# Kernel tuning notes

Hardware: AMD Instinct MI355X
Metric: run time of the kernel (lower is better)

The kernel has to match this reference:

```python
import jax, jax.numpy as jnp
import numpy as np

B, S, D, H = 8, 1024, 512, 8
HD = D // H
NEG = -1000000000.0
LN_EPS = 1e-5


def setup_inputs() -> dict:
    key = jax.random.key(0)
    ks = jax.random.split(key, 16)
    sc = 0.02
    inp = {
        "query": jax.random.normal(ks[0], (B, S, D), jnp.float32),
        "inputs": jax.random.normal(ks[1], (B, S, D), jnp.float32),
        "ren_mat": jax.random.uniform(ks[2], (B, S, S), jnp.float32) * 5.0,
        "timestamp": jax.random.normal(ks[3], (B, S, S), jnp.float32),
        # causal mask: True where attention is disallowed (strictly upper triangular)
        "mask": jnp.triu(jnp.ones((1, S, S), jnp.bool_), k=1),
        "Wq": jax.random.normal(ks[4], (D, D), jnp.float32) * sc,
        "bq": jnp.zeros((D,), jnp.float32),
        "Wk": jax.random.normal(ks[5], (D, D), jnp.float32) * sc,
        "bk": jnp.zeros((D,), jnp.float32),
        "Wv": jax.random.normal(ks[6], (D, D), jnp.float32) * sc,
        "bv": jnp.zeros((D,), jnp.float32),
        "Wo": jax.random.normal(ks[7], (D, D), jnp.float32) * sc,
        "bo": jnp.zeros((D,), jnp.float32),
        "W1": jax.random.normal(ks[8], (D, D), jnp.float32) * sc,
        "b1": jnp.zeros((D,), jnp.float32),
        "ln_g": jnp.ones((D,), jnp.float32),
        "ln_b": jnp.zeros((D,), jnp.float32),
        "l1": jax.random.uniform(ks[9], (1,), jnp.float32),
    }
    return inp


def reference(query, inputs, ren_mat, timestamp, mask,
              Wq, bq, Wk, bk, Wv, bv, Wo, bo, W1, b1, ln_g, ln_b, l1):
    # QKV projections (qk_same=False path; q,k,v all computed from `inputs`)
    def proj(x, W, b):
        return (x @ W.T + b).reshape(B, S, H, HD).transpose(0, 2, 1, 3)  # (B,H,S,HD)

    q = proj(inputs, Wq, bq)
    k = proj(inputs, Wk, bk)
    v = proj(inputs, Wv, bv)

    m = mask[:, None]  # (1,1,S,S), broadcasts over batch & heads

    scores = jnp.einsum("bhqd,bhkd->bhqk", q, k) / jnp.sqrt(jnp.float32(HD))
    scores = jnp.where(m, NEG, scores)
    prob_attn = jax.nn.softmax(scores, axis=-1)

    # memory blend: log10(ren+1) and exp(-|t|), each masked, summed, softmaxed
    ren_feat = jnp.where(m, NEG, jnp.log10(ren_mat + 1.0)[:, None])      # (B,H,S,S)
    time_stamp = jnp.where(m, NEG, jnp.exp(-jnp.abs(timestamp))[:, None])
    mem_attn = jax.nn.softmax(ren_feat + time_stamp, axis=-1)

    l = l1  # (1,) learned blend coefficient
    prob_attn = (1.0 - l) * prob_attn + l * mem_attn

    out = jnp.einsum("bhqk,bhkd->bhqd", prob_attn, v)
    out = out.transpose(0, 2, 1, 3).reshape(B, S, D)
    out = out @ Wo.T + bo

    # residual FFN + layernorm (dropout disabled / eval mode)
    out = out + (out @ W1.T + b1)
    mu = jnp.mean(out, axis=-1, keepdims=True)
    var = jnp.var(out, axis=-1, keepdims=True)
    out = (out - mu) / jnp.sqrt(var + LN_EPS) * ln_g + ln_b
    return out
```

## Files before the change

### kernel.cpp

```cpp
#include <hip/hip_runtime.h>
#include <math.h>

constexpr int kB = 8, kS = 1024, kD = 512, kH = 8, kHD = 64;
constexpr int kM = kB * kS;

typedef __attribute__((ext_vector_type(8))) short s8v;
typedef __attribute__((ext_vector_type(4))) float f4v;
typedef __attribute__((ext_vector_type(4))) unsigned short u4v;

__device__ __forceinline__ unsigned short f2bf(float f) {
    union { float f; unsigned int u; } c; c.f = f;
    unsigned int u = c.u + 0x7FFFu + ((c.u >> 16) & 1u);
    return (unsigned short)(u >> 16);
}

__device__ __forceinline__ void gl2lds(const unsigned short* g, unsigned short* l) {
    __builtin_amdgcn_global_load_lds(
        (const __attribute__((address_space(1))) unsigned int*)g,
        (__attribute__((address_space(3))) unsigned int*)l, 16, 0, 0);
}

__global__ __launch_bounds__(256) void cvt_kernel(
    const float* __restrict__ X, const float* __restrict__ Wq,
    const float* __restrict__ Wk, const float* __restrict__ Wv,
    const float* __restrict__ Wo, const float* __restrict__ W1,
    unsigned short* __restrict__ Xbf, unsigned short* __restrict__ Wqkv,
    unsigned short* __restrict__ Wobf, unsigned short* __restrict__ W1bf)
{
    const int idx = blockIdx.x * 256 + threadIdx.x;
    const float* src; unsigned short* dst; int off;
    if (idx < 1048576)      { src = X;  dst = Xbf;           off = idx; }
    else if (idx < 1114112) { src = Wq; dst = Wqkv;          off = idx - 1048576; }
    else if (idx < 1179648) { src = Wk; dst = Wqkv + 262144; off = idx - 1114112; }
    else if (idx < 1245184) { src = Wv; dst = Wqkv + 524288; off = idx - 1179648; }
    else if (idx < 1310720) { src = Wo; dst = Wobf;          off = idx - 1245184; }
    else                    { src = W1; dst = W1bf;          off = idx - 1310720; }
    const float4 v = ((const float4*)src)[off];
    u4v p;
    p[0] = f2bf(v.x); p[1] = f2bf(v.y); p[2] = f2bf(v.z); p[3] = f2bf(v.w);
    ((u4v*)dst)[off] = p;
}

__device__ __forceinline__ void mfma_core(
    const unsigned short* __restrict__ A, const unsigned short* __restrict__ B,
    unsigned short* As, unsigned short* Bs, f4v acc[4][4])
{
    const int M0 = blockIdx.x * 128, N0 = blockIdx.y * 128;
    const int t = threadIdx.x, w = t >> 6, lane = t & 63;
    const int l16 = lane & 15, quad = lane >> 4;
    const int wm = (w & 1) * 64, wn = (w >> 1) * 64;

    const unsigned short* gA[2]; const unsigned short* gB[2];
    unsigned short* lA[2]; unsigned short* lB[2];
#pragma unroll
    for (int i = 0; i < 2; ++i) {
        const int r0 = w * 32 + i * 16;
        const int r = r0 + (lane >> 2);
        const int c = (lane & 3) ^ ((r >> 1) & 3);
        gA[i] = A + (size_t)(M0 + r) * 512 + c * 8;
        gB[i] = B + (size_t)(N0 + r) * 512 + c * 8;
        lA[i] = As + r0 * 32;
        lB[i] = Bs + r0 * 32;
    }

    const f4v zero = {0.0f, 0.0f, 0.0f, 0.0f};
#pragma unroll
    for (int mt = 0; mt < 4; ++mt)
#pragma unroll
        for (int nt = 0; nt < 4; ++nt) acc[mt][nt] = zero;

#pragma unroll 1
    for (int k0 = 0; k0 < 512; k0 += 32) {
        gl2lds(gA[0] + k0, lA[0]);
        gl2lds(gA[1] + k0, lA[1]);
        gl2lds(gB[0] + k0, lB[0]);
        gl2lds(gB[1] + k0, lB[1]);
        __syncthreads();
        s8v af[4], bf_[4];
#pragma unroll
        for (int mt = 0; mt < 4; ++mt) {
            const int r = wm + mt * 16 + l16;
            const int p = r * 4 + (quad ^ ((r >> 1) & 3));
            af[mt] = *(const s8v*)&As[p * 8];
        }
#pragma unroll
        for (int nt = 0; nt < 4; ++nt) {
            const int r = wn + nt * 16 + l16;
            const int p = r * 4 + (quad ^ ((r >> 1) & 3));
            bf_[nt] = *(const s8v*)&Bs[p * 8];
        }
#pragma unroll
        for (int mt = 0; mt < 4; ++mt)
#pragma unroll
            for (int nt = 0; nt < 4; ++nt)
                acc[mt][nt] = __builtin_amdgcn_mfma_f32_16x16x32_bf16(
                    af[mt], bf_[nt], acc[mt][nt], 0, 0, 0);
        __syncthreads();
    }
}

__global__ __launch_bounds__(256) void qkv_mfma_kernel(
    const unsigned short* __restrict__ Xbf, const unsigned short* __restrict__ Wqkv,
    const float* __restrict__ bq, const float* __restrict__ bk, const float* __restrict__ bv,
    unsigned short* __restrict__ qbf, unsigned short* __restrict__ kbf,
    unsigned short* __restrict__ vTbf)
{
    __shared__ __align__(16) unsigned short As[128 * 32];
    __shared__ __align__(16) unsigned short Bs[128 * 32];
    f4v acc[4][4];
    mfma_core(Xbf, Wqkv, As, Bs, acc);

    const int M0 = blockIdx.x * 128, N0 = blockIdx.y * 128;
    const int t = threadIdx.x, w = t >> 6, lane = t & 63;
    const int l16 = lane & 15, quad = lane >> 4;
    const int wm = (w & 1) * 64, wn = (w >> 1) * 64;
    const int z = N0 >> 9;
    const float* bias = (z == 0) ? bq : (z == 1) ? bk : bv;

    if (z <= 1) {
        unsigned short* out = (z == 0) ? qbf : kbf;
#pragma unroll
        for (int nt = 0; nt < 4; ++nt) {
            const int n512 = (N0 + wn + nt * 16 + l16) & 511;
            const int h = n512 >> 6, hd = n512 & 63;
            const float bv_ = bias[n512];
#pragma unroll
            for (int mt = 0; mt < 4; ++mt) {
#pragma unroll
                for (int rr = 0; rr < 4; ++rr) {
                    const int m = M0 + wm + mt * 16 + quad * 4 + rr;
                    const int b = m >> 10, s = m & (kS - 1);
                    out[(((size_t)b * kH + h) * kS + s) * kHD + hd] =
                        f2bf(acc[mt][nt][rr] + bv_);
                }
            }
        }
    } else {
#pragma unroll
        for (int nt = 0; nt < 4; ++nt) {
            const int n512 = (N0 + wn + nt * 16 + l16) & 511;
            const int h = n512 >> 6, hd = n512 & 63;
            const float bv_ = bias[n512];
#pragma unroll
            for (int mt = 0; mt < 4; ++mt) {
                const int m0_ = M0 + wm + mt * 16 + quad * 4;
                const int b = m0_ >> 10, s = m0_ & (kS - 1);
                u4v pk;
#pragma unroll
                for (int rr = 0; rr < 4; ++rr) pk[rr] = f2bf(acc[mt][nt][rr] + bv_);
                *(u4v*)(vTbf + (((size_t)b * kH + h) * kHD + hd) * kS + s) = pk;
            }
        }
    }
}

__global__ __launch_bounds__(256) void gemm_wo_kernel(
    const unsigned short* __restrict__ Abf, const unsigned short* __restrict__ Wobf,
    const float* __restrict__ bo, float* __restrict__ out1f,
    unsigned short* __restrict__ out1bf)
{
    __shared__ __align__(16) unsigned short As[128 * 32];
    __shared__ __align__(16) unsigned short Bs[128 * 32];
    f4v acc[4][4];
    mfma_core(Abf, Wobf, As, Bs, acc);

    const int M0 = blockIdx.x * 128, N0 = blockIdx.y * 128;
    const int t = threadIdx.x, w = t >> 6, lane = t & 63;
    const int l16 = lane & 15, quad = lane >> 4;
    const int wm = (w & 1) * 64, wn = (w >> 1) * 64;
#pragma unroll
    for (int nt = 0; nt < 4; ++nt) {
        const int n = N0 + wn + nt * 16 + l16;
        const float bv_ = bo[n];
#pragma unroll
        for (int mt = 0; mt < 4; ++mt) {
#pragma unroll
            for (int rr = 0; rr < 4; ++rr) {
                const int m = M0 + wm + mt * 16 + quad * 4 + rr;
                const float val = acc[mt][nt][rr] + bv_;
                out1f[(size_t)m * kD + n] = val;
                out1bf[(size_t)m * kD + n] = f2bf(val);
            }
        }
    }
}

__global__ __launch_bounds__(256) void gemm_w1_kernel(
    const unsigned short* __restrict__ Abf, const unsigned short* __restrict__ W1bf,
    const float* __restrict__ b1, const float* __restrict__ resid,
    float* __restrict__ out)
{
    __shared__ __align__(16) unsigned short As[128 * 32];
    __shared__ __align__(16) unsigned short Bs[128 * 32];
    f4v acc[4][4];
    mfma_core(Abf, W1bf, As, Bs, acc);

    const int M0 = blockIdx.x * 128, N0 = blockIdx.y * 128;
    const int t = threadIdx.x, w = t >> 6, lane = t & 63;
    const int l16 = lane & 15, quad = lane >> 4;
    const int wm = (w & 1) * 64, wn = (w >> 1) * 64;
#pragma unroll
    for (int nt = 0; nt < 4; ++nt) {
        const int n = N0 + wn + nt * 16 + l16;
        const float bv_ = b1[n];
#pragma unroll
        for (int mt = 0; mt < 4; ++mt) {
#pragma unroll
            for (int rr = 0; rr < 4; ++rr) {
                const int m = M0 + wm + mt * 16 + quad * 4 + rr;
                out[(size_t)m * kD + n] = acc[mt][nt][rr] + bv_ + resid[(size_t)m * kD + n];
            }
        }
    }
}

__global__ __launch_bounds__(256) void mem_softmax_kernel(
    const float* __restrict__ ren, const float* __restrict__ ts,
    unsigned short* __restrict__ mem)
{
    const int bi = blockIdx.x;
    const int i = bi & (kS - 1);
    const float* renr = ren + (size_t)bi * kS;
    const float* tsr  = ts  + (size_t)bi * kS;
    unsigned short* memr = mem + (size_t)bi * kS;
    const int t = threadIdx.x;
    const int j0 = t * 4;
    __shared__ float red[4];

    const float4 r4 = *(const float4*)(renr + j0);
    const float4 t4 = *(const float4*)(tsr + j0);
    float rv[4] = {r4.x, r4.y, r4.z, r4.w};
    float tv[4] = {t4.x, t4.y, t4.z, t4.w};
    float p4[4];
    float lsum = 0.0f;
#pragma unroll
    for (int e = 0; e < 4; ++e) {
        const int j = j0 + e;
        float p = 0.0f;
        if (j <= i) {
            const float val = 0.30102999566f * __log2f(rv[e] + 1.0f) + __expf(-fabsf(tv[e]));
            p = __expf(val);
        }
        p4[e] = p;
        lsum += p;
    }
#pragma unroll
    for (int d = 1; d < 64; d <<= 1) lsum += __shfl_xor(lsum, d);
    if ((t & 63) == 0) red[t >> 6] = lsum;
    __syncthreads();
    const float Z = red[0] + red[1] + red[2] + red[3];
    const float inv = 1.0f / Z;
    u4v pk;
#pragma unroll
    for (int e = 0; e < 4; ++e) pk[e] = f2bf(p4[e] * inv);
    *(u4v*)(memr + j0) = pk;
}

#define LDSFRAG(tile, r, c) (*(const s8v*)&(tile)[(size_t)(r) * 64 + ((((c) ^ ((r) & 7))) << 3)])

__global__ __launch_bounds__(256) void flash_attn_kernel(
    const unsigned short* __restrict__ q, const unsigned short* __restrict__ k,
    const unsigned short* __restrict__ vT, const unsigned short* __restrict__ mem,
    const float* __restrict__ l1, unsigned short* __restrict__ aout)
{
    const int qt = 15 - blockIdx.x;
    const int h = blockIdx.y, b = blockIdx.z;
    const int bh = b * kH + h;
    const int t = threadIdx.x;
    const int w = t >> 6, lane = t & 63;
    const int quad = lane >> 4, l16 = lane & 15;
    const int r0 = qt * 64 + w * 16;
    const float lam = l1[0];

    __shared__ __align__(16) unsigned short KV[2][2][64 * 64];
    __shared__ __align__(16) unsigned short P_lds[4][16][72];

    const unsigned short* qrow = q + ((size_t)bh * kS + r0 + l16) * kHD;
    const s8v qa0 = *(const s8v*)(qrow + quad * 8);
    const s8v qa1 = *(const s8v*)(qrow + 32 + quad * 8);

    const unsigned short* kb = k + (size_t)bh * kS * kHD;
    const unsigned short* vb = vT + (size_t)bh * kHD * kS;
    const unsigned short* mb = mem + ((size_t)b * kS + r0 + l16) * kS;

    const unsigned short* gsrc[4];
    int gstep[4];
    unsigned short* ldst[4];
#pragma unroll
    for (int u = 0; u < 4; ++u) {
        const int s = w * 4 + u;
        const int rloc = (s & 7) * 8 + (lane >> 3);
        const int chunk = (lane & 7) ^ ((lane >> 3) & 7);
        if (s < 8) {
            gsrc[u] = kb + (size_t)rloc * kHD + chunk * 8;
            gstep[u] = kHD;
            ldst[u] = &KV[0][0][(size_t)s * 512];
        } else {
            gsrc[u] = vb + (size_t)rloc * kS + chunk * 8;
            gstep[u] = 1;
            ldst[u] = &KV[0][1][(size_t)(s - 8) * 512];
        }
    }

#pragma unroll
    for (int u = 0; u < 4; ++u) gl2lds(gsrc[u], ldst[u]);
    s8v ma0_c = *(const s8v*)(mb + quad * 8);
    s8v ma1_c = *(const s8v*)(mb + 32 + quad * 8);

    const f4v zero = {0.0f, 0.0f, 0.0f, 0.0f};
    float l_run[4] = {0.0f, 0.0f, 0.0f, 0.0f};
    f4v Oa[4], Om[4];
#pragma unroll
    for (int nt = 0; nt < 4; ++nt) { Oa[nt] = zero; Om[nt] = zero; }

    for (int kt = 0; kt <= qt; ++kt) {
        __syncthreads();
        const int cur = kt & 1;
        s8v ma0_n, ma1_n;
        if (kt < qt) {
            const int jn = (kt + 1) * 64;
            const int boff = ((kt + 1) & 1) * 8192;
#pragma unroll
            for (int u = 0; u < 4; ++u)
                gl2lds(gsrc[u] + (size_t)jn * gstep[u], ldst[u] + boff);
            ma0_n = *(const s8v*)(mb + jn + quad * 8);
            ma1_n = *(const s8v*)(mb + jn + 32 + quad * 8);
        }
        const unsigned short* Kc = &KV[cur][0][0];
        const unsigned short* Vc = &KV[cur][1][0];
        const int j0 = kt * 64;

#pragma unroll
        for (int ct = 0; ct < 4; ++ct) {
            const int r = ct * 16 + l16;
            const s8v kb0 = LDSFRAG(Kc, r, quad);
            const s8v kb1 = LDSFRAG(Kc, r, 4 + quad);
            f4v acc = zero;
            acc = __builtin_amdgcn_mfma_f32_16x16x32_bf16(qa0, kb0, acc, 0, 0, 0);
            acc = __builtin_amdgcn_mfma_f32_16x16x32_bf16(qa1, kb1, acc, 0, 0, 0);
            const int j = j0 + r;
#pragma unroll
            for (int rr = 0; rr < 4; ++rr) {
                float p = __expf(acc[rr] * 0.125f);
                if (kt == qt && j > r0 + quad * 4 + rr) p = 0.0f;
                l_run[rr] += p;
                P_lds[w][quad * 4 + rr][ct * 16 + l16] = f2bf(p);
            }
        }
        const s8v pa0 = *(const s8v*)&P_lds[w][l16][quad * 8];
        const s8v pa1 = *(const s8v*)&P_lds[w][l16][32 + quad * 8];
#pragma unroll
        for (int nt = 0; nt < 4; ++nt) {
            const int r = nt * 16 + l16;
            const s8v vb0 = LDSFRAG(Vc, r, quad);
            const s8v vb1 = LDSFRAG(Vc, r, 4 + quad);
            Oa[nt] = __builtin_amdgcn_mfma_f32_16x16x32_bf16(pa0, vb0, Oa[nt], 0, 0, 0);
            Oa[nt] = __builtin_amdgcn_mfma_f32_16x16x32_bf16(pa1, vb1, Oa[nt], 0, 0, 0);
            Om[nt] = __builtin_amdgcn_mfma_f32_16x16x32_bf16(ma0_c, vb0, Om[nt], 0, 0, 0);
            Om[nt] = __builtin_amdgcn_mfma_f32_16x16x32_bf16(ma1_c, vb1, Om[nt], 0, 0, 0);
        }
        if (kt < qt) { ma0_c = ma0_n; ma1_c = ma1_n; }
    }
    float inv[4];
#pragma unroll
    for (int rr = 0; rr < 4; ++rr) {
        float Z = l_run[rr];
        Z += __shfl_xor(Z, 1);
        Z += __shfl_xor(Z, 2);
        Z += __shfl_xor(Z, 4);
        Z += __shfl_xor(Z, 8);
        inv[rr] = (1.0f - lam) / Z;
    }
#pragma unroll
    for (int nt = 0; nt < 4; ++nt)
#pragma unroll
        for (int rr = 0; rr < 4; ++rr) {
            const int i = r0 + quad * 4 + rr;
            const int d = h * kHD + nt * 16 + l16;
            aout[((size_t)b * kS + i) * kD + d] =
                f2bf(Oa[nt][rr] * inv[rr] + lam * Om[nt][rr]);
        }
}

__global__ __launch_bounds__(256) void ln_kernel(
    const float* __restrict__ x, const float* __restrict__ g,
    const float* __restrict__ bb, float* __restrict__ out)
{
    const int row = blockIdx.x;
    const int t = threadIdx.x;
    const float* xr = x + (size_t)row * kD;
    float a = xr[t], c = xr[t + 256];
    __shared__ float red[256];
    float s1 = a + c, s2 = a * a + c * c;
    red[t] = s1;
    __syncthreads();
    for (int s = 128; s > 0; s >>= 1) {
        if (t < s) red[t] += red[t + s];
        __syncthreads();
    }
    const float sum = red[0];
    __syncthreads();
    red[t] = s2;
    __syncthreads();
    for (int s = 128; s > 0; s >>= 1) {
        if (t < s) red[t] += red[t + s];
        __syncthreads();
    }
    const float sq = red[0];
    float mu = sum * (1.0f / kD);
    float var = sq * (1.0f / kD) - mu * mu;
    float inv = rsqrtf(var + 1e-5f);
    out[(size_t)row * kD + t]       = (a - mu) * inv * g[t] + bb[t];
    out[(size_t)row * kD + t + 256] = (c - mu) * inv * g[t + 256] + bb[t + 256];
}

extern "C" void kernel_launch(void* const* d_in, const int* in_sizes, int n_in,
                              void* d_out, int out_size, void* d_ws, size_t ws_size,
                              hipStream_t stream) {
    const float* X   = (const float*)d_in[1];
    const float* ren = (const float*)d_in[2];
    const float* ts  = (const float*)d_in[3];
    const float* Wq = (const float*)d_in[5];  const float* bq = (const float*)d_in[6];
    const float* Wk = (const float*)d_in[7];  const float* bk = (const float*)d_in[8];
    const float* Wv = (const float*)d_in[9];  const float* bv = (const float*)d_in[10];
    const float* Wo = (const float*)d_in[11]; const float* bo = (const float*)d_in[12];
    const float* W1 = (const float*)d_in[13]; const float* b1 = (const float*)d_in[14];
    const float* lng = (const float*)d_in[15]; const float* lnb = (const float*)d_in[16];
    const float* l1 = (const float*)d_in[17];
    float* out = (float*)d_out;

    char* wsb = (char*)d_ws;
    unsigned short* Xbf    = (unsigned short*)(wsb);
    unsigned short* Wqkvbf = (unsigned short*)(wsb + (8u  << 20));
    unsigned short* Wobf   = (unsigned short*)(wsb + (10u << 20));
    unsigned short* W1bf   = (unsigned short*)(wsb + (11u << 20));
    unsigned short* qbf    = (unsigned short*)(wsb + (12u << 20));
    unsigned short* kbf    = (unsigned short*)(wsb + (20u << 20));
    unsigned short* vTbf   = (unsigned short*)(wsb + (28u << 20));
    unsigned short* membf  = (unsigned short*)(wsb + (36u << 20));
    unsigned short* aoutbf = (unsigned short*)(wsb + (52u << 20));
    float*          out1f  = (float*)(wsb + (60u << 20));
    unsigned short* out1bf = (unsigned short*)(wsb + (76u << 20));

    cvt_kernel<<<dim3(5376), 256, 0, stream>>>(
        X, Wq, Wk, Wv, Wo, W1, Xbf, Wqkvbf, Wobf, W1bf);
    qkv_mfma_kernel<<<dim3(kM / 128, 1536 / 128), 256, 0, stream>>>(
        Xbf, Wqkvbf, bq, bk, bv, qbf, kbf, vTbf);
    mem_softmax_kernel<<<dim3(kB * kS), 256, 0, stream>>>(ren, ts, membf);
    flash_attn_kernel<<<dim3(kS / 64, kH, kB), 256, 0, stream>>>(
        qbf, kbf, vTbf, membf, l1, aoutbf);
    gemm_wo_kernel<<<dim3(kM / 128, kD / 128), 256, 0, stream>>>(
        aoutbf, Wobf, bo, out1f, out1bf);
    gemm_w1_kernel<<<dim3(kM / 128, kD / 128), 256, 0, stream>>>(
        out1bf, W1bf, b1, out1f, out);
    ln_kernel<<<dim3(kM), 256, 0, stream>>>(out, lng, lnb, out);
}
```

Baseline: 283.2 us.

## Fuse prep kernels, fold residual into W1, pair causal tiles in attention

Merges the weight/input conversion and the memory-softmax into one launch. Adds the identity to W1 so the residual is computed inside the GEMM, which removes the fp32 out1 buffer and its reads. The V projection is computed transposed so each store goes directly into the vT layout. Flash attention now gives each block one high and one low query tile to balance causal work, sharing K/V loads and halving the grid. The Wo and W1 GEMMs switch to 128x64 tiles to launch more blocks. Folding the residual into bf16 W1 rounds the identity term to bf16, which adds precision risk.

```diff
diff --git a/kernel.cpp b/kernel.cpp
--- a/kernel.cpp
+++ b/kernel.cpp
@@ -20,46 +20,98 @@
         (__attribute__((address_space(3))) unsigned int*)l, 16, 0, 0);
 }
 
-__global__ __launch_bounds__(256) void cvt_kernel(
+__global__ __launch_bounds__(256) void prep_kernel(
     const float* __restrict__ X, const float* __restrict__ Wq,
     const float* __restrict__ Wk, const float* __restrict__ Wv,
     const float* __restrict__ Wo, const float* __restrict__ W1,
+    const float* __restrict__ ren, const float* __restrict__ ts,
     unsigned short* __restrict__ Xbf, unsigned short* __restrict__ Wqkv,
-    unsigned short* __restrict__ Wobf, unsigned short* __restrict__ W1bf)
-{
-    const int idx = blockIdx.x * 256 + threadIdx.x;
-    const float* src; unsigned short* dst; int off;
-    if (idx < 1048576)      { src = X;  dst = Xbf;           off = idx; }
-    else if (idx < 1114112) { src = Wq; dst = Wqkv;          off = idx - 1048576; }
-    else if (idx < 1179648) { src = Wk; dst = Wqkv + 262144; off = idx - 1114112; }
-    else if (idx < 1245184) { src = Wv; dst = Wqkv + 524288; off = idx - 1179648; }
-    else if (idx < 1310720) { src = Wo; dst = Wobf;          off = idx - 1245184; }
-    else                    { src = W1; dst = W1bf;          off = idx - 1310720; }
-    const float4 v = ((const float4*)src)[off];
-    u4v p;
-    p[0] = f2bf(v.x); p[1] = f2bf(v.y); p[2] = f2bf(v.z); p[3] = f2bf(v.w);
-    ((u4v*)dst)[off] = p;
-}
-
-__device__ __forceinline__ void mfma_core(
+    unsigned short* __restrict__ Wobf, unsigned short* __restrict__ W1bf,
+    unsigned short* __restrict__ mem)
+{
+    __shared__ float red[4];
+    const int t = threadIdx.x;
+    if (blockIdx.x < 5376) {
+        const int idx = blockIdx.x * 256 + t;
+        const float* src; unsigned short* dst; int off; bool isw1 = false;
+        if (idx < 1048576)      { src = X;  dst = Xbf;           off = idx; }
+        else if (idx < 1114112) { src = Wq; dst = Wqkv;          off = idx - 1048576; }
+        else if (idx < 1179648) { src = Wk; dst = Wqkv + 262144; off = idx - 1114112; }
+        else if (idx < 1245184) { src = Wv; dst = Wqkv + 524288; off = idx - 1179648; }
+        else if (idx < 1310720) { src = Wo; dst = Wobf;          off = idx - 1245184; }
+        else                    { src = W1; dst = W1bf;          off = idx - 1310720; isw1 = true; }
+        float4 v = ((const float4*)src)[off];
+        if (isw1) {
+            const int e0 = off * 4;
+            const int row = e0 >> 9, col0 = e0 & 511;
+            if (row >= col0 && row < col0 + 4) ((float*)&v)[row - col0] += 1.0f;
+        }
+        u4v p;
+        p[0] = f2bf(v.x); p[1] = f2bf(v.y); p[2] = f2bf(v.z); p[3] = f2bf(v.w);
+        ((u4v*)dst)[off] = p;
+        return;
+    }
+    const int bi = blockIdx.x - 5376;
+    const int i = bi & (kS - 1);
+    const float* renr = ren + (size_t)bi * kS;
+    const float* tsr  = ts  + (size_t)bi * kS;
+    unsigned short* memr = mem + (size_t)bi * kS;
+    const int j0 = t * 4;
+    const float4 r4 = *(const float4*)(renr + j0);
+    const float4 t4 = *(const float4*)(tsr + j0);
+    float rv[4] = {r4.x, r4.y, r4.z, r4.w};
+    float tv[4] = {t4.x, t4.y, t4.z, t4.w};
+    float p4[4];
+    float lsum = 0.0f;
+#pragma unroll
+    for (int e = 0; e < 4; ++e) {
+        const int j = j0 + e;
+        float p = 0.0f;
+        if (j <= i) {
+            const float val = 0.30102999566f * __log2f(rv[e] + 1.0f) + __expf(-fabsf(tv[e]));
+            p = __expf(val);
+        }
+        p4[e] = p;
+        lsum += p;
+    }
+#pragma unroll
+    for (int d = 1; d < 64; d <<= 1) lsum += __shfl_xor(lsum, d);
+    if ((t & 63) == 0) red[t >> 6] = lsum;
+    __syncthreads();
+    const float Z = red[0] + red[1] + red[2] + red[3];
+    const float inv = 1.0f / Z;
+    u4v pk;
+#pragma unroll
+    for (int e = 0; e < 4; ++e) pk[e] = f2bf(p4[e] * inv);
+    *(u4v*)(memr + j0) = pk;
+}
+
+template <int NT>
+__device__ __forceinline__ void mfma_core2(
     const unsigned short* __restrict__ A, const unsigned short* __restrict__ B,
-    unsigned short* As, unsigned short* Bs, f4v acc[4][4])
-{
-    const int M0 = blockIdx.x * 128, N0 = blockIdx.y * 128;
+    int M0, int N0, unsigned short* As, unsigned short* Bs, f4v (&acc)[4][NT])
+{
     const int t = threadIdx.x, w = t >> 6, lane = t & 63;
     const int l16 = lane & 15, quad = lane >> 4;
-    const int wm = (w & 1) * 64, wn = (w >> 1) * 64;
-
-    const unsigned short* gA[2]; const unsigned short* gB[2];
-    unsigned short* lA[2]; unsigned short* lB[2];
+    const int wm = (w & 1) * 64, wn = (w >> 1) * (NT * 16);
+    constexpr int NB = NT / 2;
+
+    const unsigned short* gA[2]; unsigned short* lA[2];
 #pragma unroll
     for (int i = 0; i < 2; ++i) {
         const int r0 = w * 32 + i * 16;
         const int r = r0 + (lane >> 2);
         const int c = (lane & 3) ^ ((r >> 1) & 3);
         gA[i] = A + (size_t)(M0 + r) * 512 + c * 8;
+        lA[i] = As + r0 * 32;
+    }
+    const unsigned short* gB[NB]; unsigned short* lB[NB];
+#pragma unroll
+    for (int i = 0; i < NB; ++i) {
+        const int r0 = w * (16 * NB) + i * 16;
+        const int r = r0 + (lane >> 2);
+        const int c = (lane & 3) ^ ((r >> 1) & 3);
         gB[i] = B + (size_t)(N0 + r) * 512 + c * 8;
-        lA[i] = As + r0 * 32;
         lB[i] = Bs + r0 * 32;
     }
 
@@ -67,16 +119,16 @@
 #pragma unroll
     for (int mt = 0; mt < 4; ++mt)
 #pragma unroll
-        for (int nt = 0; nt < 4; ++nt) acc[mt][nt] = zero;
+        for (int nt = 0; nt < NT; ++nt) acc[mt][nt] = zero;
 
 #pragma unroll 1
     for (int k0 = 0; k0 < 512; k0 += 32) {
         gl2lds(gA[0] + k0, lA[0]);
         gl2lds(gA[1] + k0, lA[1]);
-        gl2lds(gB[0] + k0, lB[0]);
-        gl2lds(gB[1] + k0, lB[1]);
+#pragma unroll
+        for (int i = 0; i < NB; ++i) gl2lds(gB[i] + k0, lB[i]);
         __syncthreads();
-        s8v af[4], bf_[4];
+        s8v af[4], bf_[NT];
 #pragma unroll
         for (int mt = 0; mt < 4; ++mt) {
             const int r = wm + mt * 16 + l16;
@@ -84,7 +136,7 @@
             af[mt] = *(const s8v*)&As[p * 8];
         }
 #pragma unroll
-        for (int nt = 0; nt < 4; ++nt) {
+        for (int nt = 0; nt < NT; ++nt) {
             const int r = wn + nt * 16 + l16;
             const int p = r * 4 + (quad ^ ((r >> 1) & 3));
             bf_[nt] = *(const s8v*)&Bs[p * 8];
@@ -92,7 +144,7 @@
 #pragma unroll
         for (int mt = 0; mt < 4; ++mt)
 #pragma unroll
-            for (int nt = 0; nt < 4; ++nt)
+            for (int nt = 0; nt < NT; ++nt)
                 acc[mt][nt] = __builtin_amdgcn_mfma_f32_16x16x32_bf16(
                     af[mt], bf_[nt], acc[mt][nt], 0, 0, 0);
         __syncthreads();
@@ -108,16 +160,16 @@
     __shared__ __align__(16) unsigned short As[128 * 32];
     __shared__ __align__(16) unsigned short Bs[128 * 32];
     f4v acc[4][4];
-    mfma_core(Xbf, Wqkv, As, Bs, acc);
-
-    const int M0 = blockIdx.x * 128, N0 = blockIdx.y * 128;
+    const int y = blockIdx.y;
     const int t = threadIdx.x, w = t >> 6, lane = t & 63;
     const int l16 = lane & 15, quad = lane >> 4;
     const int wm = (w & 1) * 64, wn = (w >> 1) * 64;
-    const int z = N0 >> 9;
-    const float* bias = (z == 0) ? bq : (z == 1) ? bk : bv;
-
-    if (z <= 1) {
+
+    if (y < 8) {
+        const int M0 = blockIdx.x * 128, N0 = y * 128;
+        mfma_core2<4>(Xbf, Wqkv, M0, N0, As, Bs, acc);
+        const int z = N0 >> 9;
+        const float* bias = (z == 0) ? bq : bk;
         unsigned short* out = (z == 0) ? qbf : kbf;
 #pragma unroll
         for (int nt = 0; nt < 4; ++nt) {
@@ -136,19 +188,22 @@
             }
         }
     } else {
-#pragma unroll
-        for (int nt = 0; nt < 4; ++nt) {
-            const int n512 = (N0 + wn + nt * 16 + l16) & 511;
-            const int h = n512 >> 6, hd = n512 & 63;
-            const float bv_ = bias[n512];
-#pragma unroll
-            for (int mt = 0; mt < 4; ++mt) {
-                const int m0_ = M0 + wm + mt * 16 + quad * 4;
-                const int b = m0_ >> 10, s = m0_ & (kS - 1);
-                u4v pk;
-#pragma unroll
-                for (int rr = 0; rr < 4; ++rr) pk[rr] = f2bf(acc[mt][nt][rr] + bv_);
-                *(u4v*)(vTbf + (((size_t)b * kH + h) * kHD + hd) * kS + s) = pk;
+        const int M0 = (y - 8) * 128, N0 = blockIdx.x * 128;
+        mfma_core2<4>(Wqkv + (size_t)1024 * 512, Xbf, M0, N0, As, Bs, acc);
+#pragma unroll
+        for (int mt = 0; mt < 4; ++mt) {
+#pragma unroll
+            for (int rr = 0; rr < 4; ++rr) {
+                const int vcol = M0 + wm + mt * 16 + quad * 4 + rr;
+                const int h = vcol >> 6, hd = vcol & 63;
+                const float bv_ = bv[vcol];
+#pragma unroll
+                for (int nt = 0; nt < 4; ++nt) {
+                    const int sg = N0 + wn + nt * 16 + l16;
+                    const int b = sg >> 10, s = sg & (kS - 1);
+                    vTbf[(((size_t)b * kH + h) * kHD + hd) * kS + s] =
+                        f2bf(acc[mt][nt][rr] + bv_);
+                }
             }
         }
     }
@@ -156,104 +211,54 @@
 
 __global__ __launch_bounds__(256) void gemm_wo_kernel(
     const unsigned short* __restrict__ Abf, const unsigned short* __restrict__ Wobf,
-    const float* __restrict__ bo, float* __restrict__ out1f,
-    unsigned short* __restrict__ out1bf)
+    const float* __restrict__ bo, unsigned short* __restrict__ out1bf)
 {
     __shared__ __align__(16) unsigned short As[128 * 32];
-    __shared__ __align__(16) unsigned short Bs[128 * 32];
-    f4v acc[4][4];
-    mfma_core(Abf, Wobf, As, Bs, acc);
-
-    const int M0 = blockIdx.x * 128, N0 = blockIdx.y * 128;
+    __shared__ __align__(16) unsigned short Bs[64 * 32];
+    f4v acc[4][2];
+    const int M0 = blockIdx.x * 128, N0 = blockIdx.y * 64;
+    mfma_core2<2>(Abf, Wobf, M0, N0, As, Bs, acc);
     const int t = threadIdx.x, w = t >> 6, lane = t & 63;
     const int l16 = lane & 15, quad = lane >> 4;
-    const int wm = (w & 1) * 64, wn = (w >> 1) * 64;
-#pragma unroll
-    for (int nt = 0; nt < 4; ++nt) {
+    const int wm = (w & 1) * 64, wn = (w >> 1) * 32;
+#pragma unroll
+    for (int nt = 0; nt < 2; ++nt) {
         const int n = N0 + wn + nt * 16 + l16;
         const float bv_ = bo[n];
 #pragma unroll
-        for (int mt = 0; mt < 4; ++mt) {
+        for (int mt = 0; mt < 4; ++mt)
 #pragma unroll
             for (int rr = 0; rr < 4; ++rr) {
                 const int m = M0 + wm + mt * 16 + quad * 4 + rr;
-                const float val = acc[mt][nt][rr] + bv_;
-                out1f[(size_t)m * kD + n] = val;
-                out1bf[(size_t)m * kD + n] = f2bf(val);
-            }
-        }
+                out1bf[(size_t)m * kD + n] = f2bf(acc[mt][nt][rr] + bv_);
+            }
     }
 }
 
 __global__ __launch_bounds__(256) void gemm_w1_kernel(
     const unsigned short* __restrict__ Abf, const unsigned short* __restrict__ W1bf,
-    const float* __restrict__ b1, const float* __restrict__ resid,
-    float* __restrict__ out)
+    const float* __restrict__ b1, float* __restrict__ out)
 {
     __shared__ __align__(16) unsigned short As[128 * 32];
-    __shared__ __align__(16) unsigned short Bs[128 * 32];
-    f4v acc[4][4];
-    mfma_core(Abf, W1bf, As, Bs, acc);
-
-    const int M0 = blockIdx.x * 128, N0 = blockIdx.y * 128;
+    __shared__ __align__(16) unsigned short Bs[64 * 32];
+    f4v acc[4][2];
+    const int M0 = blockIdx.x * 128, N0 = blockIdx.y * 64;
+    mfma_core2<2>(Abf, W1bf, M0, N0, As, Bs, acc);
     const int t = threadIdx.x, w = t >> 6, lane = t & 63;
     const int l16 = lane & 15, quad = lane >> 4;
-    const int wm = (w & 1) * 64, wn = (w >> 1) * 64;
-#pragma unroll
-    for (int nt = 0; nt < 4; ++nt) {
+    const int wm = (w & 1) * 64, wn = (w >> 1) * 32;
+#pragma unroll
+    for (int nt = 0; nt < 2; ++nt) {
         const int n = N0 + wn + nt * 16 + l16;
         const float bv_ = b1[n];
 #pragma unroll
-        for (int mt = 0; mt < 4; ++mt) {
+        for (int mt = 0; mt < 4; ++mt)
 #pragma unroll
             for (int rr = 0; rr < 4; ++rr) {
                 const int m = M0 + wm + mt * 16 + quad * 4 + rr;
-                out[(size_t)m * kD + n] = acc[mt][nt][rr] + bv_ + resid[(size_t)m * kD + n];
-            }
-        }
-    }
-}
-
-__global__ __launch_bounds__(256) void mem_softmax_kernel(
-    const float* __restrict__ ren, const float* __restrict__ ts,
-    unsigned short* __restrict__ mem)
-{
-    const int bi = blockIdx.x;
-    const int i = bi & (kS - 1);
-    const float* renr = ren + (size_t)bi * kS;
-    const float* tsr  = ts  + (size_t)bi * kS;
-    unsigned short* memr = mem + (size_t)bi * kS;
-    const int t = threadIdx.x;
-    const int j0 = t * 4;
-    __shared__ float red[4];
-
-    const float4 r4 = *(const float4*)(renr + j0);
-    const float4 t4 = *(const float4*)(tsr + j0);
-    float rv[4] = {r4.x, r4.y, r4.z, r4.w};
-    float tv[4] = {t4.x, t4.y, t4.z, t4.w};
-    float p4[4];
-    float lsum = 0.0f;
-#pragma unroll
-    for (int e = 0; e < 4; ++e) {
-        const int j = j0 + e;
-        float p = 0.0f;
-        if (j <= i) {
-            const float val = 0.30102999566f * __log2f(rv[e] + 1.0f) + __expf(-fabsf(tv[e]));
-            p = __expf(val);
-        }
-        p4[e] = p;
-        lsum += p;
-    }
-#pragma unroll
-    for (int d = 1; d < 64; d <<= 1) lsum += __shfl_xor(lsum, d);
-    if ((t & 63) == 0) red[t >> 6] = lsum;
-    __syncthreads();
-    const float Z = red[0] + red[1] + red[2] + red[3];
-    const float inv = 1.0f / Z;
-    u4v pk;
-#pragma unroll
-    for (int e = 0; e < 4; ++e) pk[e] = f2bf(p4[e] * inv);
-    *(u4v*)(memr + j0) = pk;
+                out[(size_t)m * kD + n] = acc[mt][nt][rr] + bv_;
+            }
+    }
 }
 
 #define LDSFRAG(tile, r, c) (*(const s8v*)&(tile)[(size_t)(r) * 64 + ((((c) ^ ((r) & 7))) << 3)])
@@ -263,25 +268,31 @@
     const unsigned short* __restrict__ vT, const unsigned short* __restrict__ mem,
     const float* __restrict__ l1, unsigned short* __restrict__ aout)
 {
-    const int qt = 15 - blockIdx.x;
+    const int qp = blockIdx.x;
+    const int hi = 15 - qp, lo = qp;
     const int h = blockIdx.y, b = blockIdx.z;
     const int bh = b * kH + h;
     const int t = threadIdx.x;
     const int w = t >> 6, lane = t & 63;
     const int quad = lane >> 4, l16 = lane & 15;
-    const int r0 = qt * 64 + w * 16;
     const float lam = l1[0];
 
     __shared__ __align__(16) unsigned short KV[2][2][64 * 64];
     __shared__ __align__(16) unsigned short P_lds[4][16][72];
 
-    const unsigned short* qrow = q + ((size_t)bh * kS + r0 + l16) * kHD;
-    const s8v qa0 = *(const s8v*)(qrow + quad * 8);
-    const s8v qa1 = *(const s8v*)(qrow + 32 + quad * 8);
+    const int tbase[2] = {hi * 64, lo * 64};
+    s8v qa[2][2];
+    const unsigned short* mbase[2];
+#pragma unroll
+    for (int ti = 0; ti < 2; ++ti) {
+        const unsigned short* qrow = q + ((size_t)bh * kS + tbase[ti] + w * 16 + l16) * kHD;
+        qa[ti][0] = *(const s8v*)(qrow + quad * 8);
+        qa[ti][1] = *(const s8v*)(qrow + 32 + quad * 8);
+        mbase[ti] = mem + ((size_t)b * kS + tbase[ti] + w * 16 + l16) * kS;
+    }
 
     const unsigned short* kb = k + (size_t)bh * kS * kHD;
     const unsigned short* vb = vT + (size_t)bh * kHD * kS;
-    const unsigned short* mb = mem + ((size_t)b * kS + r0 + l16) * kS;
 
     const unsigned short* gsrc[4];
     int gstep[4];
@@ -304,82 +315,111 @@
 
 #pragma unroll
     for (int u = 0; u < 4; ++u) gl2lds(gsrc[u], ldst[u]);
-    s8v ma0_c = *(const s8v*)(mb + quad * 8);
-    s8v ma1_c = *(const s8v*)(mb + 32 + quad * 8);
+    s8v maC[2][2];
+#pragma unroll
+    for (int ti = 0; ti < 2; ++ti) {
+        maC[ti][0] = *(const s8v*)(mbase[ti] + quad * 8);
+        maC[ti][1] = *(const s8v*)(mbase[ti] + 32 + quad * 8);
+    }
 
     const f4v zero = {0.0f, 0.0f, 0.0f, 0.0f};
-    float l_run[4] = {0.0f, 0.0f, 0.0f, 0.0f};
-    f4v Oa[4], Om[4];
-#pragma unroll
-    for (int nt = 0; nt < 4; ++nt) { Oa[nt] = zero; Om[nt] = zero; }
-
-    for (int kt = 0; kt <= qt; ++kt) {
+    f4v Oa[2][4], Om[2][4];
+    float lr[2][4];
+#pragma unroll
+    for (int ti = 0; ti < 2; ++ti)
+#pragma unroll
+        for (int nt = 0; nt < 4; ++nt) {
+            Oa[ti][nt] = zero; Om[ti][nt] = zero; lr[ti][nt] = 0.0f;
+        }
+
+    for (int kt = 0; kt <= hi; ++kt) {
         __syncthreads();
         const int cur = kt & 1;
-        s8v ma0_n, ma1_n;
-        if (kt < qt) {
+        s8v maN[2][2];
+        const bool stage_next = (kt < hi);
+        if (stage_next) {
             const int jn = (kt + 1) * 64;
             const int boff = ((kt + 1) & 1) * 8192;
 #pragma unroll
             for (int u = 0; u < 4; ++u)
                 gl2lds(gsrc[u] + (size_t)jn * gstep[u], ldst[u] + boff);
-            ma0_n = *(const s8v*)(mb + jn + quad * 8);
-            ma1_n = *(const s8v*)(mb + jn + 32 + quad * 8);
+            maN[0][0] = *(const s8v*)(mbase[0] + jn + quad * 8);
+            maN[0][1] = *(const s8v*)(mbase[0] + jn + 32 + quad * 8);
+            if (kt + 1 <= lo) {
+                maN[1][0] = *(const s8v*)(mbase[1] + jn + quad * 8);
+                maN[1][1] = *(const s8v*)(mbase[1] + jn + 32 + quad * 8);
+            }
         }
         const unsigned short* Kc = &KV[cur][0][0];
         const unsigned short* Vc = &KV[cur][1][0];
-        const int j0 = kt * 64;
-
-#pragma unroll
-        for (int ct = 0; ct < 4; ++ct) {
-            const int r = ct * 16 + l16;
-            const s8v kb0 = LDSFRAG(Kc, r, quad);
-            const s8v kb1 = LDSFRAG(Kc, r, 4 + quad);
-            f4v acc = zero;
-            acc = __builtin_amdgcn_mfma_f32_16x16x32_bf16(qa0, kb0, acc, 0, 0, 0);
-            acc = __builtin_amdgcn_mfma_f32_16x16x32_bf16(qa1, kb1, acc, 0, 0, 0);
-            const int j = j0 + r;
-#pragma unroll
-            for (int rr = 0; rr < 4; ++rr) {
-                float p = __expf(acc[rr] * 0.125f);
-                if (kt == qt && j > r0 + quad * 4 + rr) p = 0.0f;
-                l_run[rr] += p;
-                P_lds[w][quad * 4 + rr][ct * 16 + l16] = f2bf(p);
-            }
-        }
-        const s8v pa0 = *(const s8v*)&P_lds[w][l16][quad * 8];
-        const s8v pa1 = *(const s8v*)&P_lds[w][l16][32 + quad * 8];
+
+        s8v vf[4][2];
 #pragma unroll
         for (int nt = 0; nt < 4; ++nt) {
             const int r = nt * 16 + l16;
-            const s8v vb0 = LDSFRAG(Vc, r, quad);
-            const s8v vb1 = LDSFRAG(Vc, r, 4 + quad);
-            Oa[nt] = __builtin_amdgcn_mfma_f32_16x16x32_bf16(pa0, vb0, Oa[nt], 0, 0, 0);
-            Oa[nt] = __builtin_amdgcn_mfma_f32_16x16x32_bf16(pa1, vb1, Oa[nt], 0, 0, 0);
-            Om[nt] = __builtin_amdgcn_mfma_f32_16x16x32_bf16(ma0_c, vb0, Om[nt], 0, 0, 0);
-            Om[nt] = __builtin_amdgcn_mfma_f32_16x16x32_bf16(ma1_c, vb1, Om[nt], 0, 0, 0);
-        }
-        if (kt < qt) { ma0_c = ma0_n; ma1_c = ma1_n; }
-    }
-    float inv[4];
-#pragma unroll
-    for (int rr = 0; rr < 4; ++rr) {
-        float Z = l_run[rr];
-        Z += __shfl_xor(Z, 1);
-        Z += __shfl_xor(Z, 2);
-        Z += __shfl_xor(Z, 4);
-        Z += __shfl_xor(Z, 8);
-        inv[rr] = (1.0f - lam) / Z;
-    }
-#pragma unroll
-    for (int nt = 0; nt < 4; ++nt)
+            vf[nt][0] = LDSFRAG(Vc, r, quad);
+            vf[nt][1] = LDSFRAG(Vc, r, 4 + quad);
+        }
+
+#pragma unroll
+        for (int ti = 0; ti < 2; ++ti) {
+            if (ti == 1 && kt > lo) continue;
+            const bool diag = (kt == ((ti == 0) ? hi : lo));
+#pragma unroll
+            for (int ct = 0; ct < 4; ++ct) {
+                const int r = ct * 16 + l16;
+                const s8v kb0 = LDSFRAG(Kc, r, quad);
+                const s8v kb1 = LDSFRAG(Kc, r, 4 + quad);
+                f4v acc = zero;
+                acc = __builtin_amdgcn_mfma_f32_16x16x32_bf16(qa[ti][0], kb0, acc, 0, 0, 0);
+                acc = __builtin_amdgcn_mfma_f32_16x16x32_bf16(qa[ti][1], kb1, acc, 0, 0, 0);
+#pragma unroll
+                for (int rr = 0; rr < 4; ++rr) {
+                    float p = __expf(acc[rr] * 0.125f);
+                    if (diag && (ct * 16 + l16) > (w * 16 + quad * 4 + rr)) p = 0.0f;
+                    lr[ti][rr] += p;
+                    P_lds[w][quad * 4 + rr][ct * 16 + l16] = f2bf(p);
+                }
+            }
+            const s8v pa0 = *(const s8v*)&P_lds[w][l16][quad * 8];
+            const s8v pa1 = *(const s8v*)&P_lds[w][l16][32 + quad * 8];
+#pragma unroll
+            for (int nt = 0; nt < 4; ++nt) {
+                Oa[ti][nt] = __builtin_amdgcn_mfma_f32_16x16x32_bf16(pa0, vf[nt][0], Oa[ti][nt], 0, 0, 0);
+                Oa[ti][nt] = __builtin_amdgcn_mfma_f32_16x16x32_bf16(pa1, vf[nt][1], Oa[ti][nt], 0, 0, 0);
+                Om[ti][nt] = __builtin_amdgcn_mfma_f32_16x16x32_bf16(maC[ti][0], vf[nt][0], Om[ti][nt], 0, 0, 0);
+                Om[ti][nt] = __builtin_amdgcn_mfma_f32_16x16x32_bf16(maC[ti][1], vf[nt][1], Om[ti][nt], 0, 0, 0);
+            }
+        }
+        if (stage_next) {
+            maC[0][0] = maN[0][0]; maC[0][1] = maN[0][1];
+            if (kt + 1 <= lo) { maC[1][0] = maN[1][0]; maC[1][1] = maN[1][1]; }
+        }
+    }
+
+#pragma unroll
+    for (int ti = 0; ti < 2; ++ti) {
+        float inv[4];
 #pragma unroll
         for (int rr = 0; rr < 4; ++rr) {
-            const int i = r0 + quad * 4 + rr;
-            const int d = h * kHD + nt * 16 + l16;
-            aout[((size_t)b * kS + i) * kD + d] =
-                f2bf(Oa[nt][rr] * inv[rr] + lam * Om[nt][rr]);
-        }
+            float Z = lr[ti][rr];
+            Z += __shfl_xor(Z, 1);
+            Z += __shfl_xor(Z, 2);
+            Z += __shfl_xor(Z, 4);
+            Z += __shfl_xor(Z, 8);
+            inv[rr] = (1.0f - lam) / Z;
+        }
+        const int r0 = tbase[ti] + w * 16;
+#pragma unroll
+        for (int nt = 0; nt < 4; ++nt)
+#pragma unroll
+            for (int rr = 0; rr < 4; ++rr) {
+                const int i = r0 + quad * 4 + rr;
+                const int d = h * kHD + nt * 16 + l16;
+                aout[((size_t)b * kS + i) * kD + d] =
+                    f2bf(Oa[ti][nt][rr] * inv[rr] + lam * Om[ti][nt][rr]);
+            }
+    }
 }
 
 __global__ __launch_bounds__(256) void ln_kernel(
@@ -439,19 +479,17 @@
     unsigned short* vTbf   = (unsigned short*)(wsb + (28u << 20));
     unsigned short* membf  = (unsigned short*)(wsb + (36u << 20));
     unsigned short* aoutbf = (unsigned short*)(wsb + (52u << 20));
-    float*          out1f  = (float*)(wsb + (60u << 20));
-    unsigned short* out1bf = (unsigned short*)(wsb + (76u << 20));
-
-    cvt_kernel<<<dim3(5376), 256, 0, stream>>>(
-        X, Wq, Wk, Wv, Wo, W1, Xbf, Wqkvbf, Wobf, W1bf);
-    qkv_mfma_kernel<<<dim3(kM / 128, 1536 / 128), 256, 0, stream>>>(
+    unsigned short* out1bf = (unsigned short*)(wsb + (60u << 20));
+
+    prep_kernel<<<dim3(5376 + kB * kS), 256, 0, stream>>>(
+        X, Wq, Wk, Wv, Wo, W1, ren, ts, Xbf, Wqkvbf, Wobf, W1bf, membf);
+    qkv_mfma_kernel<<<dim3(kM / 128, 12), 256, 0, stream>>>(
         Xbf, Wqkvbf, bq, bk, bv, qbf, kbf, vTbf);
-    mem_softmax_kernel<<<dim3(kB * kS), 256, 0, stream>>>(ren, ts, membf);
-    flash_attn_kernel<<<dim3(kS / 64, kH, kB), 256, 0, stream>>>(
+    flash_attn_kernel<<<dim3(8, kH, kB), 256, 0, stream>>>(
         qbf, kbf, vTbf, membf, l1, aoutbf);
-    gemm_wo_kernel<<<dim3(kM / 128, kD / 128), 256, 0, stream>>>(
-        aoutbf, Wobf, bo, out1f, out1bf);
-    gemm_w1_kernel<<<dim3(kM / 128, kD / 128), 256, 0, stream>>>(
-        out1bf, W1bf, b1, out1f, out);
+    gemm_wo_kernel<<<dim3(kM / 128, kD / 64), 256, 0, stream>>>(
+        aoutbf, Wobf, bo, out1bf);
+    gemm_w1_kernel<<<dim3(kM / 128, kD / 64), 256, 0, stream>>>(
+        out1bf, W1bf, b1, out);
     ln_kernel<<<dim3(kM), 256, 0, stream>>>(out, lng, lnb, out);
 }
```

Result: faster. 275.4 us (-2.8%).
